# Kernel optimization log

Hardware: AMD Instinct MI355X
Metric: run time of the kernel (lower is better)

## Reference

```python
import jax, jax.numpy as jnp
import numpy as np

D_MODEL = 1024
NUM_HEADS = 16
B, S = 2, 2048


def setup_inputs() -> dict:
    key = jax.random.key(0)
    ks = jax.random.split(key, 11)
    scale = 1.0 / np.sqrt(D_MODEL)
    inp = {
        'q': jax.random.normal(ks[0], (B, S, D_MODEL), jnp.float32),
        'k': jax.random.normal(ks[1], (B, S, D_MODEL), jnp.float32),
        'v': jax.random.normal(ks[2], (B, S, D_MODEL), jnp.float32),
        'w_q': jax.random.normal(ks[3], (D_MODEL, D_MODEL), jnp.float32) * scale,
        'b_q': jax.random.normal(ks[4], (D_MODEL,), jnp.float32) * 0.01,
        'w_k': jax.random.normal(ks[5], (D_MODEL, D_MODEL), jnp.float32) * scale,
        'b_k': jax.random.normal(ks[6], (D_MODEL,), jnp.float32) * 0.01,
        'w_v': jax.random.normal(ks[7], (D_MODEL, D_MODEL), jnp.float32) * scale,
        'b_v': jax.random.normal(ks[8], (D_MODEL,), jnp.float32) * 0.01,
        'w_o': jax.random.normal(ks[9], (D_MODEL, D_MODEL), jnp.float32) * scale,
        'b_o': jax.random.normal(ks[10], (D_MODEL,), jnp.float32) * 0.01,
    }
    return inp


def reference(q, k, v, w_q, b_q, w_k, b_k, w_v, b_v, w_o, b_o):
    Bq, Sq, D = q.shape
    H = NUM_HEADS
    dh = D // H
    # projections (weights stored as [in, out])
    query = q @ w_q + b_q
    key = k @ w_k + b_k
    value = v @ w_v + b_v
    # [B, S, D] -> [B, H, S, dh]
    query = query.reshape(Bq, Sq, H, dh).transpose(0, 2, 1, 3)
    key = key.reshape(Bq, -1, H, dh).transpose(0, 2, 1, 3)
    value = value.reshape(Bq, -1, H, dh).transpose(0, 2, 1, 3)
    # NOTE: original module does NOT scale by 1/sqrt(dh)
    scores = jnp.einsum('bhqd,bhkd->bhqk', query, key)  # [B,H,S,S]
    causal_mask = jnp.triu(jnp.ones((Sq, Sq), dtype=bool), k=1)  # True above diag
    scores = jnp.where(causal_mask[None, None], -jnp.inf, scores)
    attn = jax.nn.softmax(scores, axis=-1)
    data = jnp.einsum('bhqk,bhkd->bhqd', attn, value)  # [B,H,S,dh]
    # FAITHFUL to original bug: transpose(0,1) then view(B, S, -1)
    data = data.transpose(1, 0, 2, 3).reshape(Bq, Sq, -1)  # [H,B,S,dh] -> [B,S,D]
    return data @ w_o + b_o
```

## Files before the change

kernel.cpp:

```cpp
#include <hip/hip_runtime.h>

typedef __fp16 f16;
typedef __fp16 f16x8 __attribute__((ext_vector_type(8)));
typedef __fp16 f16x4 __attribute__((ext_vector_type(4)));
typedef __fp16 f16x2 __attribute__((ext_vector_type(2)));
typedef float f32x4 __attribute__((ext_vector_type(4)));
typedef float f32x16 __attribute__((ext_vector_type(16)));

#define D_MODEL 1024
#define SEQ 2048
#define NH 16
#define MTOT 4096

typedef const __attribute__((address_space(1))) unsigned int* gp1_t;
typedef __attribute__((address_space(3))) unsigned int* lp3_t;

__device__ __forceinline__ void gload_lds16(const void* g, void* l) {
  __builtin_amdgcn_global_load_lds((gp1_t)g, (lp3_t)l, 16, 0, 0);
}

__device__ __forceinline__ int permrow(int r) {
  int bp = r >> 11, u = (r >> 7) & 15, t = r & 127;
  int g16 = (bp << 4) | u;
  return ((((g16 & 1) << 4) | (g16 >> 1)) << 7) + t;
}

__device__ __forceinline__ unsigned int pkrtz(float a, float b) {
  union { f16x2 h; unsigned int u; } z;
  z.h = __builtin_amdgcn_cvt_pkrtz(a, b);
  return z.u;
}

__global__ __launch_bounds__(256) void cvt_all(const float* __restrict__ q,
                                               const float* __restrict__ k,
                                               const float* __restrict__ v,
                                               const float* __restrict__ wq,
                                               const float* __restrict__ wk,
                                               const float* __restrict__ wv,
                                               const float* __restrict__ wo,
                                               f16* __restrict__ qkv16,
                                               f16* __restrict__ wT) {
  __shared__ float tl[64][65];
  int bid = blockIdx.x, tid = threadIdx.x;
  if (bid < 6144) {
    int i = bid * 256 + tid;
    const int NT = (MTOT * D_MODEL) / 8;
    const float* src;
    int t;
    if (i < NT) { src = q; t = i; }
    else if (i < 2 * NT) { src = k; t = i - NT; }
    else { src = v; t = i - 2 * NT; }
    const float4* s4 = (const float4*)src;
    float4 a = s4[2 * t], b = s4[2 * t + 1];
    f16x8 h;
    h[0] = (f16)a.x; h[1] = (f16)a.y; h[2] = (f16)a.z; h[3] = (f16)a.w;
    h[4] = (f16)b.x; h[5] = (f16)b.y; h[6] = (f16)b.z; h[7] = (f16)b.w;
    *(f16x8*)(qkv16 + (size_t)i * 8) = h;
  } else {
    int bb = bid - 6144;
    int mat = bb >> 8, tile = bb & 255;
    int tk = (tile >> 4) << 6, tn = (tile & 15) << 6;
    const float* W = mat == 0 ? wq : mat == 1 ? wk : mat == 2 ? wv : wo;
    int rr = tid >> 4, c4 = (tid & 15) << 2;
#pragma unroll
    for (int it = 0; it < 4; ++it) {
      const float* p = W + (size_t)(tk + it * 16 + rr) * D_MODEL + tn + c4;
      float4 val = *(const float4*)p;
      tl[it * 16 + rr][c4 + 0] = val.x;
      tl[it * 16 + rr][c4 + 1] = val.y;
      tl[it * 16 + rr][c4 + 2] = val.z;
      tl[it * 16 + rr][c4 + 3] = val.w;
    }
    __syncthreads();
    int n = tid & 63, kseg = (tid >> 6) << 4;
    f16x8 lo, hi;
#pragma unroll
    for (int j = 0; j < 8; ++j) lo[j] = (f16)tl[kseg + j][n];
#pragma unroll
    for (int j = 0; j < 8; ++j) hi[j] = (f16)tl[kseg + 8 + j][n];
    f16* d = wT + (size_t)mat * (D_MODEL * D_MODEL) + (size_t)(tn + n) * D_MODEL + tk + kseg;
    *(f16x8*)d = lo;
    *(f16x8*)(d + 8) = hi;
  }
}

#define SLOT_Q 8192
__global__ __launch_bounds__(256, 2) void gemm_qkv(const f16* __restrict__ q16,
                                                   const f16* __restrict__ k16,
                                                   const f16* __restrict__ v16,
                                                   const f16* __restrict__ wT,
                                                   const float* __restrict__ bq,
                                                   const float* __restrict__ bk,
                                                   const float* __restrict__ bv,
                                                   f16* __restrict__ Q16,
                                                   f16* __restrict__ K16,
                                                   f16* __restrict__ VT16) {
  extern __shared__ __attribute__((aligned(16))) f16 sm[];
  const int K = D_MODEL, N = D_MODEL;
  const size_t WEL = (size_t)D_MODEL * D_MODEL;
  int z = blockIdx.z;
  const f16* A = z == 0 ? q16 : z == 1 ? k16 : v16;
  const f16* BT = wT + (size_t)z * WEL;
  const float* bias = z == 0 ? bq : z == 1 ? bk : bv;

  int tid = threadIdx.x;
  int w = tid >> 6, lane = tid & 63;
  int g = lane >> 4, c = lane & 15;
  int wr = w >> 1, wc = w & 1;
  int m0 = blockIdx.x * 128, n0 = blockIdx.y * 128;
  f32x4 acc[4][4] = {};

  int sl0 = lane >> 3, s = lane & 7;
  int u = s ^ sl0;
  int rlow = u >> 2, gsl = u & 3;
  const f16* Agp = A + (size_t)(m0 + w * 32 + 2 * sl0 + rlow) * K + gsl * 8;
  const f16* Bgp = BT + (size_t)(n0 + w * 32 + 2 * sl0 + rlow) * K + gsl * 8;

#define STAGE_Q(tt, bi)                                                      \
  {                                                                          \
    f16* dA = sm + (bi)*SLOT_Q + w * 1024;                                   \
    f16* dB = sm + (bi)*SLOT_Q + 4096 + w * 1024;                            \
    const f16* sa = Agp + (size_t)(tt)*32;                                   \
    const f16* sb = Bgp + (size_t)(tt)*32;                                   \
    gload_lds16(sa, dA);                                                     \
    gload_lds16(sa + (size_t)16 * K, dA + 512);                              \
    gload_lds16(sb, dB);                                                     \
    gload_lds16(sb + (size_t)16 * K, dB + 512);                              \
  }

  STAGE_Q(0, 0)
  STAGE_Q(1, 1)
  STAGE_Q(2, 2)

  const int NKT = K / 32;
  for (int t = 0; t < NKT; ++t) {
    if (t < NKT - 2) asm volatile("s_waitcnt vmcnt(8)" ::: "memory");
    else if (t == NKT - 2) asm volatile("s_waitcnt vmcnt(4)" ::: "memory");
    else asm volatile("s_waitcnt vmcnt(0)" ::: "memory");
    __builtin_amdgcn_sched_barrier(0);
    __builtin_amdgcn_s_barrier();
    __builtin_amdgcn_sched_barrier(0);
    if (t + 3 < NKT) STAGE_Q(t + 3, (t + 3) & 3)

    const char* Ac = (const char*)(sm + (t & 3) * SLOT_Q);
    const char* Bc = Ac + 8192;
    f16x8 af[4], bf[4];
#pragma unroll
    for (int mi = 0; mi < 4; ++mi) {
      int row = wr * 64 + mi * 16 + c;
      int tb = (row >> 1) * 128 + (((((row & 1) << 2) | g) ^ ((row >> 1) & 7)) << 4);
      af[mi] = *(const f16x8*)(Ac + tb);
    }
#pragma unroll
    for (int ni = 0; ni < 4; ++ni) {
      int row = wc * 64 + ni * 16 + c;
      int tb = (row >> 1) * 128 + (((((row & 1) << 2) | g) ^ ((row >> 1) & 7)) << 4);
      bf[ni] = *(const f16x8*)(Bc + tb);
    }
    asm volatile("s_waitcnt lgkmcnt(0)" ::: "memory");
    __builtin_amdgcn_sched_barrier(0);
    __builtin_amdgcn_s_setprio(1);
#pragma unroll
    for (int mi = 0; mi < 4; ++mi)
#pragma unroll
      for (int ni = 0; ni < 4; ++ni)
        acc[mi][ni] = __builtin_amdgcn_mfma_f32_16x16x32_f16(af[mi], bf[ni], acc[mi][ni], 0, 0, 0);
    __builtin_amdgcn_s_setprio(0);
  }

  int rb = m0 + wr * 64;
  int cb = n0 + wc * 64;
  if (z < 2) {
    f16* O = z == 0 ? Q16 : K16;
#pragma unroll
    for (int m = 0; m < 4; ++m) {
      int row0 = rb + m * 16 + 4 * g;
#pragma unroll
      for (int n = 0; n < 4; ++n) {
        int col = cb + n * 16 + c;
        float bv2 = bias[col];
#pragma unroll
        for (int r = 0; r < 4; ++r) O[(size_t)(row0 + r) * N + col] = (f16)(acc[m][n][r] + bv2);
      }
    }
  } else {
    f16* O = VT16;
#pragma unroll
    for (int m = 0; m < 4; ++m) {
      int s0f = rb + m * 16 + 4 * g;
      int bb = s0f >> 11, ss = s0f & (SEQ - 1);
#pragma unroll
      for (int n = 0; n < 4; ++n) {
        int col = cb + n * 16 + c;
        float bv2 = bias[col];
        f16x4 hv;
#pragma unroll
        for (int r = 0; r < 4; ++r) hv[r] = (f16)(acc[m][n][r] + bv2);
        *(f16x4*)(O + ((size_t)(bb * NH + (col >> 6)) * 64 + (col & 63)) * SEQ + ss) = hv;
      }
    }
  }
}

__global__ __launch_bounds__(256, 2) void gemm_out(const f16* __restrict__ A,
                                                   const f16* __restrict__ BT,
                                                   const float* __restrict__ bias,
                                                   float* __restrict__ O) {
  const int K = D_MODEL, N = D_MODEL;
  __shared__ f16 As[64 * 64];
  __shared__ f16 Bs[128 * 64];
  int tid = threadIdx.x;
  int w = tid >> 6, lane = tid & 63;
  int g = lane >> 4, c = lane & 15;
  int wr = w >> 1, wc = w & 1;
  int m0 = blockIdx.x * 64, n0 = blockIdx.y * 128;
  f32x4 acc[2][4] = {};

  for (int kt = 0; kt < K; kt += 64) {
#pragma unroll
    for (int i = 0; i < 2; ++i) {
      int seg = w * 2 + i;
      int p = seg * 1024 + lane * 16;
      int row = p >> 7;
      int colb = (p & 127) ^ ((row & 7) << 4);
      int ae = kt + (colb >> 1);
      gload_lds16(A + (size_t)permrow(m0 + row) * K + ae, &As[seg * 512]);
    }
#pragma unroll
    for (int i = 0; i < 4; ++i) {
      int seg = w * 4 + i;
      int p = seg * 1024 + lane * 16;
      int row = p >> 7;
      int colb = (p & 127) ^ ((row & 7) << 4);
      int ae = kt + (colb >> 1);
      gload_lds16(BT + (size_t)(n0 + row) * K + ae, &Bs[seg * 512]);
    }
    __syncthreads();
    f16x8 af[2][2], bf[4][2];
#pragma unroll
    for (int m = 0; m < 2; ++m) {
#pragma unroll
      for (int kk = 0; kk < 2; ++kk) {
        int row = wr * 32 + m * 16 + c;
        int tb = (row * 128 + kk * 64 + g * 16) ^ ((row & 7) << 4);
        af[m][kk] = *(const f16x8*)((const char*)As + tb);
      }
    }
#pragma unroll
    for (int n = 0; n < 4; ++n) {
#pragma unroll
      for (int kk = 0; kk < 2; ++kk) {
        int row = wc * 64 + n * 16 + c;
        int tb = (row * 128 + kk * 64 + g * 16) ^ ((row & 7) << 4);
        bf[n][kk] = *(const f16x8*)((const char*)Bs + tb);
      }
    }
    __builtin_amdgcn_s_setprio(1);
#pragma unroll
    for (int m = 0; m < 2; ++m)
#pragma unroll
      for (int n = 0; n < 4; ++n)
#pragma unroll
        for (int kk = 0; kk < 2; ++kk)
          acc[m][n] = __builtin_amdgcn_mfma_f32_16x16x32_f16(af[m][kk], bf[n][kk], acc[m][n], 0, 0, 0);
    __builtin_amdgcn_s_setprio(0);
    __syncthreads();
  }

  int rb = m0 + wr * 32;
  int cb = n0 + wc * 64;
#pragma unroll
  for (int m = 0; m < 2; ++m) {
    int row0 = rb + m * 16 + 4 * g;
#pragma unroll
    for (int n = 0; n < 4; ++n) {
      int col = cb + n * 16 + c;
      float bv = bias[col];
#pragma unroll
      for (int r = 0; r < 4; ++r) O[(size_t)(row0 + r) * N + col] = acc[m][n][r] + bv;
    }
  }
}

#define THR2 11.5f
__global__ __launch_bounds__(256, 2) void attn_kernel(const f16* __restrict__ Q,
                                                      const f16* __restrict__ K,
                                                      const f16* __restrict__ VT,
                                                      f16* __restrict__ AO) {
  __shared__ __attribute__((aligned(16))) f16 Ksh[2][2][64 * 64];
  __shared__ __attribute__((aligned(16))) f16 Vsh[2][2][64 * 64];
  const int BUFO = 2 * 64 * 64;
  int tid = threadIdx.x;
  int w = tid >> 6, lane = tid & 63;
  int c = lane & 31, hi = lane >> 5;
  int qh = w & 1, par = w >> 1;
  int blk = blockIdx.x;
  int bh = blk & 31;
  int uu = blk >> 5;
  int cb = 31 - uu;
  int b = bh >> 4, h = bh & 15;
  int q0 = cb * 64 + qh * 32;
  const int NT = cb + 1;
  const size_t brow = (size_t)b * SEQ;
  const int hcol = h * 64;

  int sr = lane >> 3;
  int seo = ((lane & 7) ^ sr) << 3;
  const f16* Kgb = K + (size_t)(brow + qh * 32 + sr) * D_MODEL + hcol + seo;
  const f16* Vgb = VT + ((size_t)bh * 64 + qh * 32 + sr) * SEQ + seo;
  f16* Kshf = &Ksh[0][0][0];
  f16* Vshf = &Vsh[0][0][0];
  f16* KshW = Kshf + par * 4096 + qh * 32 * 64;
  f16* VshW = Vshf + par * 4096 + qh * 32 * 64;

  const f16 LOG2E = (f16)1.44269504f;
  f16x8 qf[4];
  const f16* Qp = Q + (size_t)(brow + q0 + c) * D_MODEL + hcol + 8 * hi;
#pragma unroll
  for (int kk = 0; kk < 4; ++kk) {
    qf[kk] = *(const f16x8*)(Qp + 16 * kk);
#pragma unroll
    for (int j = 0; j < 8; ++j) qf[kk][j] = (f16)(qf[kk][j] * LOG2E);
  }

  float m_st = -1e30f, l_st = 0.f;
  f32x16 o0 = {}, o1 = {};

  if (par < NT) {
    int kv = par * 64;
#pragma unroll
    for (int j = 0; j < 4; ++j) {
      gload_lds16(Kgb + (size_t)(kv + j * 8) * D_MODEL, KshW + (j * 8) * 64);
      gload_lds16(Vgb + (size_t)(j * 8) * SEQ + kv, VshW + (j * 8) * 64);
    }
  }
  __syncthreads();

  int rsw = (c & 7) << 4;
  int cur = 0;
  const int U = (NT + 1) >> 1;
  for (int u = 0; u < U; ++u) {
    int tpre = 2 * u + 2 + par;
    if (tpre < NT) {
      int kv = tpre * 64;
      f16* kd = KshW + (cur ^ 1) * BUFO;
      f16* vd = VshW + (cur ^ 1) * BUFO;
#pragma unroll
      for (int j = 0; j < 4; ++j) {
        gload_lds16(Kgb + (size_t)(kv + j * 8) * D_MODEL, kd + (j * 8) * 64);
        gload_lds16(Vgb + (size_t)(j * 8) * SEQ + kv, vd + (j * 8) * 64);
      }
    }
    int t = 2 * u + par;
    if (t < NT) {
      const char* Kb = (const char*)(Kshf + cur * BUFO + par * 4096);
      const char* Vb = (const char*)(Vshf + cur * BUFO + par * 4096);
      f16x8 kf[2][4];
#pragma unroll
      for (int ks = 0; ks < 2; ++ks)
#pragma unroll
        for (int kk = 0; kk < 4; ++kk)
          kf[ks][kk] = *(const f16x8*)(Kb + (((ks * 32 + c) * 128 + 32 * kk + 16 * hi) ^ rsw));
      f32x16 s0 = {}, s1 = {};
      __builtin_amdgcn_s_setprio(1);
#pragma unroll
      for (int kk = 0; kk < 4; ++kk) {
        s0 = __builtin_amdgcn_mfma_f32_32x32x16_f16(kf[0][kk], qf[kk], s0, 0, 0, 0);
        s1 = __builtin_amdgcn_mfma_f32_32x32x16_f16(kf[1][kk], qf[kk], s1, 0, 0, 0);
      }
      __builtin_amdgcn_s_setprio(0);
      f16x8 vf[2][4];
#pragma unroll
      for (int dt = 0; dt < 2; ++dt)
#pragma unroll
        for (int kk = 0; kk < 4; ++kk)
          vf[dt][kk] = *(const f16x8*)(Vb + (((dt * 32 + c) * 128 + 32 * kk + 16 * hi) ^ rsw));
      if (t == NT - 1) {
        int q = q0 + c;
        int kvb = t * 64 + 4 * hi;
#pragma unroll
        for (int r = 0; r < 16; ++r) {
          int kv = kvb + (r & 3) + 8 * (r >> 2);
          if (kv > q) s0[r] = -1e30f;
          if (kv + 32 > q) s1[r] = -1e30f;
        }
      }
      float t8[8];
#pragma unroll
      for (int r = 0; r < 8; ++r)
        t8[r] = fmaxf(fmaxf(s0[r], s0[r + 8]), fmaxf(s1[r], s1[r + 8]));
      float pm = fmaxf(fmaxf(fmaxf(t8[0], t8[1]), fmaxf(t8[2], t8[3])),
                       fmaxf(fmaxf(t8[4], t8[5]), fmaxf(t8[6], t8[7])));
      float mx = fmaxf(pm, __shfl_xor(pm, 32));
      if (__any(mx > m_st + THR2)) {
        float mnew = fmaxf(m_st, mx);
        float corr = __builtin_amdgcn_exp2f(m_st - mnew);
        l_st *= corr;
#pragma unroll
        for (int r = 0; r < 16; ++r) { o0[r] *= corr; o1[r] *= corr; }
        m_st = mnew;
      }
      float ts[16];
#pragma unroll
      for (int r = 0; r < 16; ++r) {
        float p0 = __builtin_amdgcn_exp2f(s0[r] - m_st);
        float p1 = __builtin_amdgcn_exp2f(s1[r] - m_st);
        s0[r] = p0; s1[r] = p1;
        ts[r] = p0 + p1;
      }
#pragma unroll
      for (int st = 8; st > 0; st >>= 1)
#pragma unroll
        for (int r = 0; r < st; ++r) ts[r] += ts[r + st];
      l_st += ts[0];
      union PU { unsigned int u[4]; f16x8 v; };
      PU pu[4];
#pragma unroll
      for (int kk = 0; kk < 4; ++kk) {
        int rb = 8 * (kk & 1);
        unsigned int la0, la1, lb0, lb1;
        if (kk < 2) {
          la0 = pkrtz(s0[rb + 0], s0[rb + 1]);
          la1 = pkrtz(s0[rb + 2], s0[rb + 3]);
          lb0 = pkrtz(s0[rb + 4], s0[rb + 5]);
          lb1 = pkrtz(s0[rb + 6], s0[rb + 7]);
        } else {
          la0 = pkrtz(s1[rb + 0], s1[rb + 1]);
          la1 = pkrtz(s1[rb + 2], s1[rb + 3]);
          lb0 = pkrtz(s1[rb + 4], s1[rb + 5]);
          lb1 = pkrtz(s1[rb + 6], s1[rb + 7]);
        }
        asm("v_permlane32_swap_b32 %0, %1" : "+v"(la0), "+v"(lb0));
        asm("v_permlane32_swap_b32 %0, %1" : "+v"(la1), "+v"(lb1));
        pu[kk].u[0] = la0; pu[kk].u[1] = la1; pu[kk].u[2] = lb0; pu[kk].u[3] = lb1;
      }
      __builtin_amdgcn_s_setprio(1);
#pragma unroll
      for (int kk = 0; kk < 4; ++kk) {
        o0 = __builtin_amdgcn_mfma_f32_32x32x16_f16(vf[0][kk], pu[kk].v, o0, 0, 0, 0);
        o1 = __builtin_amdgcn_mfma_f32_32x32x16_f16(vf[1][kk], pu[kk].v, o1, 0, 0, 0);
      }
      __builtin_amdgcn_s_setprio(0);
    }
    __syncthreads();
    cur ^= 1;
  }

  float* sc = (float*)Kshf;
  int mb = (qh * 64 + lane) * 34;
  if (par == 1) {
    sc[mb] = m_st;
    sc[mb + 1] = l_st;
#pragma unroll
    for (int r = 0; r < 16; ++r) { sc[mb + 2 + r] = o0[r]; sc[mb + 18 + r] = o1[r]; }
  }
  __syncthreads();
  if (par == 0) {
    float m1 = sc[mb], l1 = sc[mb + 1];
    float mm = fmaxf(m_st, m1);
    float c0 = __builtin_amdgcn_exp2f(m_st - mm);
    float c1 = __builtin_amdgcn_exp2f(m1 - mm);
    float l = l_st * c0 + l1 * c1;
#pragma unroll
    for (int r = 0; r < 16; ++r) {
      o0[r] = o0[r] * c0 + sc[mb + 2 + r] * c1;
      o1[r] = o1[r] * c0 + sc[mb + 18 + r] * c1;
    }
    float lt = l + __shfl_xor(l, 32);
    float linv = 1.0f / lt;
    f16* aoq = AO + ((size_t)bh * SEQ + q0 + c) * 64 + 4 * hi;
#pragma unroll
    for (int rq = 0; rq < 4; ++rq) {
      f16x4 h0, h1;
#pragma unroll
      for (int r = 0; r < 4; ++r) {
        h0[r] = (f16)(o0[4 * rq + r] * linv);
        h1[r] = (f16)(o1[4 * rq + r] * linv);
      }
      *(f16x4*)(aoq + 8 * rq) = h0;
      *(f16x4*)(aoq + 32 + 8 * rq) = h1;
    }
  }
}

extern "C" void kernel_launch(void* const* d_in, const int* in_sizes, int n_in,
                              void* d_out, int out_size, void* d_ws, size_t ws_size,
                              hipStream_t stream) {
  const float* q  = (const float*)d_in[0];
  const float* k  = (const float*)d_in[1];
  const float* v  = (const float*)d_in[2];
  const float* wq = (const float*)d_in[3];
  const float* bq = (const float*)d_in[4];
  const float* wk = (const float*)d_in[5];
  const float* bk = (const float*)d_in[6];
  const float* wv = (const float*)d_in[7];
  const float* bv = (const float*)d_in[8];
  const float* wo = (const float*)d_in[9];
  const float* bo = (const float*)d_in[10];

  const size_t TEN = (size_t)MTOT * D_MODEL;
  const size_t WEL = (size_t)D_MODEL * D_MODEL;
  f16* ws  = (f16*)d_ws;
  f16* q16 = ws;
  f16* k16 = q16 + TEN;
  f16* v16 = k16 + TEN;
  f16* wT  = v16 + TEN;
  f16* Q16 = wT + 4 * WEL;
  f16* K16 = Q16 + TEN;
  f16* VT16 = K16 + TEN;
  f16* AO  = q16;

  static bool attr_set = false;
  if (!attr_set) {
    hipFuncSetAttribute(reinterpret_cast<const void*>(&gemm_qkv),
                        hipFuncAttributeMaxDynamicSharedMemorySize, 65536);
    attr_set = true;
  }

  cvt_all<<<7168, 256, 0, stream>>>(q, k, v, wq, wk, wv, wo, q16, wT);
  gemm_qkv<<<dim3(32, 8, 3), 256, 65536, stream>>>(q16, k16, v16, wT, bq, bk, bv, Q16, K16, VT16);
  attn_kernel<<<1024, 256, 0, stream>>>(Q16, K16, VT16, AO);
  gemm_out<<<dim3(64, 8), 256, 0, stream>>>(AO, wT + 3 * WEL, bo, (float*)d_out);
}
```

Measured before the change: 108.4 us.

## Load K/V fragments directly from global memory, dropping LDS double buffering

The attention kernel no longer stages K and V tiles through double-buffered shared memory with async global-to-LDS loads and per-iteration barriers. Each wave now reads its K and V MFMA fragments straight from global memory (relying on L2/L1 for reuse across the two q-half waves), and only a small float scratch array remains for the final merge. Launch bounds are raised to allow three blocks per CU. In exchange, K/V reuse across waves becomes redundant global traffic and load latency is no longer hidden by explicit prefetching.

```diff
diff --git a/kernel.cpp b/kernel.cpp
--- a/kernel.cpp
+++ b/kernel.cpp
@@ -283,13 +283,11 @@
 }
 
 #define THR2 11.5f
-__global__ __launch_bounds__(256, 2) void attn_kernel(const f16* __restrict__ Q,
+__global__ __launch_bounds__(256, 3) void attn_kernel(const f16* __restrict__ Q,
                                                       const f16* __restrict__ K,
                                                       const f16* __restrict__ VT,
                                                       f16* __restrict__ AO) {
-  __shared__ __attribute__((aligned(16))) f16 Ksh[2][2][64 * 64];
-  __shared__ __attribute__((aligned(16))) f16 Vsh[2][2][64 * 64];
-  const int BUFO = 2 * 64 * 64;
+  __shared__ float sc[128 * 34];
   int tid = threadIdx.x;
   int w = tid >> 6, lane = tid & 63;
   int c = lane & 31, hi = lane >> 5;
@@ -304,14 +302,8 @@
   const size_t brow = (size_t)b * SEQ;
   const int hcol = h * 64;
 
-  int sr = lane >> 3;
-  int seo = ((lane & 7) ^ sr) << 3;
-  const f16* Kgb = K + (size_t)(brow + qh * 32 + sr) * D_MODEL + hcol + seo;
-  const f16* Vgb = VT + ((size_t)bh * 64 + qh * 32 + sr) * SEQ + seo;
-  f16* Kshf = &Ksh[0][0][0];
-  f16* Vshf = &Vsh[0][0][0];
-  f16* KshW = Kshf + par * 4096 + qh * 32 * 64;
-  f16* VshW = Vshf + par * 4096 + qh * 32 * 64;
+  const f16* Kl = K + (size_t)(brow + c) * D_MODEL + hcol + 8 * hi;
+  const f16* Vl = VT + ((size_t)bh * 64 + c) * SEQ + 8 * hi;
 
   const f16 LOG2E = (f16)1.44269504f;
   f16x8 qf[4];
@@ -326,127 +318,99 @@
   float m_st = -1e30f, l_st = 0.f;
   f32x16 o0 = {}, o1 = {};
 
-  if (par < NT) {
-    int kv = par * 64;
-#pragma unroll
-    for (int j = 0; j < 4; ++j) {
-      gload_lds16(Kgb + (size_t)(kv + j * 8) * D_MODEL, KshW + (j * 8) * 64);
-      gload_lds16(Vgb + (size_t)(j * 8) * SEQ + kv, VshW + (j * 8) * 64);
-    }
-  }
-  __syncthreads();
-
-  int rsw = (c & 7) << 4;
-  int cur = 0;
-  const int U = (NT + 1) >> 1;
-  for (int u = 0; u < U; ++u) {
-    int tpre = 2 * u + 2 + par;
-    if (tpre < NT) {
-      int kv = tpre * 64;
-      f16* kd = KshW + (cur ^ 1) * BUFO;
-      f16* vd = VshW + (cur ^ 1) * BUFO;
-#pragma unroll
-      for (int j = 0; j < 4; ++j) {
-        gload_lds16(Kgb + (size_t)(kv + j * 8) * D_MODEL, kd + (j * 8) * 64);
-        gload_lds16(Vgb + (size_t)(j * 8) * SEQ + kv, vd + (j * 8) * 64);
-      }
-    }
-    int t = 2 * u + par;
-    if (t < NT) {
-      const char* Kb = (const char*)(Kshf + cur * BUFO + par * 4096);
-      const char* Vb = (const char*)(Vshf + cur * BUFO + par * 4096);
-      f16x8 kf[2][4];
-#pragma unroll
-      for (int ks = 0; ks < 2; ++ks)
-#pragma unroll
-        for (int kk = 0; kk < 4; ++kk)
-          kf[ks][kk] = *(const f16x8*)(Kb + (((ks * 32 + c) * 128 + 32 * kk + 16 * hi) ^ rsw));
-      f32x16 s0 = {}, s1 = {};
-      __builtin_amdgcn_s_setprio(1);
-#pragma unroll
-      for (int kk = 0; kk < 4; ++kk) {
-        s0 = __builtin_amdgcn_mfma_f32_32x32x16_f16(kf[0][kk], qf[kk], s0, 0, 0, 0);
-        s1 = __builtin_amdgcn_mfma_f32_32x32x16_f16(kf[1][kk], qf[kk], s1, 0, 0, 0);
-      }
-      __builtin_amdgcn_s_setprio(0);
-      f16x8 vf[2][4];
-#pragma unroll
-      for (int dt = 0; dt < 2; ++dt)
-#pragma unroll
-        for (int kk = 0; kk < 4; ++kk)
-          vf[dt][kk] = *(const f16x8*)(Vb + (((dt * 32 + c) * 128 + 32 * kk + 16 * hi) ^ rsw));
-      if (t == NT - 1) {
-        int q = q0 + c;
-        int kvb = t * 64 + 4 * hi;
-#pragma unroll
-        for (int r = 0; r < 16; ++r) {
-          int kv = kvb + (r & 3) + 8 * (r >> 2);
-          if (kv > q) s0[r] = -1e30f;
-          if (kv + 32 > q) s1[r] = -1e30f;
-        }
-      }
-      float t8[8];
-#pragma unroll
-      for (int r = 0; r < 8; ++r)
-        t8[r] = fmaxf(fmaxf(s0[r], s0[r + 8]), fmaxf(s1[r], s1[r + 8]));
-      float pm = fmaxf(fmaxf(fmaxf(t8[0], t8[1]), fmaxf(t8[2], t8[3])),
-                       fmaxf(fmaxf(t8[4], t8[5]), fmaxf(t8[6], t8[7])));
-      float mx = fmaxf(pm, __shfl_xor(pm, 32));
-      if (__any(mx > m_st + THR2)) {
-        float mnew = fmaxf(m_st, mx);
-        float corr = __builtin_amdgcn_exp2f(m_st - mnew);
-        l_st *= corr;
-#pragma unroll
-        for (int r = 0; r < 16; ++r) { o0[r] *= corr; o1[r] *= corr; }
-        m_st = mnew;
-      }
-      float ts[16];
+  for (int t = par; t < NT; t += 2) {
+    int kv0 = t * 64;
+    const f16* K0 = Kl + (size_t)kv0 * D_MODEL;
+    const f16* K1 = K0 + (size_t)32 * D_MODEL;
+    const f16* V0 = Vl + kv0;
+    const f16* V1 = V0 + (size_t)32 * SEQ;
+    f16x8 kf[2][4], vf[2][4];
+#pragma unroll
+    for (int kk = 0; kk < 4; ++kk) {
+      kf[0][kk] = *(const f16x8*)(K0 + 16 * kk);
+      kf[1][kk] = *(const f16x8*)(K1 + 16 * kk);
+    }
+#pragma unroll
+    for (int kk = 0; kk < 4; ++kk) {
+      vf[0][kk] = *(const f16x8*)(V0 + 16 * kk);
+      vf[1][kk] = *(const f16x8*)(V1 + 16 * kk);
+    }
+    f32x16 s0 = {}, s1 = {};
+    __builtin_amdgcn_s_setprio(1);
+#pragma unroll
+    for (int kk = 0; kk < 4; ++kk) {
+      s0 = __builtin_amdgcn_mfma_f32_32x32x16_f16(kf[0][kk], qf[kk], s0, 0, 0, 0);
+      s1 = __builtin_amdgcn_mfma_f32_32x32x16_f16(kf[1][kk], qf[kk], s1, 0, 0, 0);
+    }
+    __builtin_amdgcn_s_setprio(0);
+    if (t == NT - 1) {
+      int q = q0 + c;
+      int kvb = t * 64 + 4 * hi;
 #pragma unroll
       for (int r = 0; r < 16; ++r) {
-        float p0 = __builtin_amdgcn_exp2f(s0[r] - m_st);
-        float p1 = __builtin_amdgcn_exp2f(s1[r] - m_st);
-        s0[r] = p0; s1[r] = p1;
-        ts[r] = p0 + p1;
-      }
-#pragma unroll
-      for (int st = 8; st > 0; st >>= 1)
-#pragma unroll
-        for (int r = 0; r < st; ++r) ts[r] += ts[r + st];
-      l_st += ts[0];
-      union PU { unsigned int u[4]; f16x8 v; };
-      PU pu[4];
-#pragma unroll
-      for (int kk = 0; kk < 4; ++kk) {
-        int rb = 8 * (kk & 1);
-        unsigned int la0, la1, lb0, lb1;
-        if (kk < 2) {
-          la0 = pkrtz(s0[rb + 0], s0[rb + 1]);
-          la1 = pkrtz(s0[rb + 2], s0[rb + 3]);
-          lb0 = pkrtz(s0[rb + 4], s0[rb + 5]);
-          lb1 = pkrtz(s0[rb + 6], s0[rb + 7]);
-        } else {
-          la0 = pkrtz(s1[rb + 0], s1[rb + 1]);
-          la1 = pkrtz(s1[rb + 2], s1[rb + 3]);
-          lb0 = pkrtz(s1[rb + 4], s1[rb + 5]);
-          lb1 = pkrtz(s1[rb + 6], s1[rb + 7]);
-        }
-        asm("v_permlane32_swap_b32 %0, %1" : "+v"(la0), "+v"(lb0));
-        asm("v_permlane32_swap_b32 %0, %1" : "+v"(la1), "+v"(lb1));
-        pu[kk].u[0] = la0; pu[kk].u[1] = la1; pu[kk].u[2] = lb0; pu[kk].u[3] = lb1;
-      }
-      __builtin_amdgcn_s_setprio(1);
-#pragma unroll
-      for (int kk = 0; kk < 4; ++kk) {
-        o0 = __builtin_amdgcn_mfma_f32_32x32x16_f16(vf[0][kk], pu[kk].v, o0, 0, 0, 0);
-        o1 = __builtin_amdgcn_mfma_f32_32x32x16_f16(vf[1][kk], pu[kk].v, o1, 0, 0, 0);
-      }
-      __builtin_amdgcn_s_setprio(0);
-    }
-    __syncthreads();
-    cur ^= 1;
-  }
-
-  float* sc = (float*)Kshf;
+        int kv = kvb + (r & 3) + 8 * (r >> 2);
+        if (kv > q) s0[r] = -1e30f;
+        if (kv + 32 > q) s1[r] = -1e30f;
+      }
+    }
+    float t8[8];
+#pragma unroll
+    for (int r = 0; r < 8; ++r)
+      t8[r] = fmaxf(fmaxf(s0[r], s0[r + 8]), fmaxf(s1[r], s1[r + 8]));
+    float pm = fmaxf(fmaxf(fmaxf(t8[0], t8[1]), fmaxf(t8[2], t8[3])),
+                     fmaxf(fmaxf(t8[4], t8[5]), fmaxf(t8[6], t8[7])));
+    float mx = fmaxf(pm, __shfl_xor(pm, 32));
+    if (__any(mx > m_st + THR2)) {
+      float mnew = fmaxf(m_st, mx);
+      float corr = __builtin_amdgcn_exp2f(m_st - mnew);
+      l_st *= corr;
+#pragma unroll
+      for (int r = 0; r < 16; ++r) { o0[r] *= corr; o1[r] *= corr; }
+      m_st = mnew;
+    }
+    float ts[16];
+#pragma unroll
+    for (int r = 0; r < 16; ++r) {
+      float p0 = __builtin_amdgcn_exp2f(s0[r] - m_st);
+      float p1 = __builtin_amdgcn_exp2f(s1[r] - m_st);
+      s0[r] = p0; s1[r] = p1;
+      ts[r] = p0 + p1;
+    }
+#pragma unroll
+    for (int st = 8; st > 0; st >>= 1)
+#pragma unroll
+      for (int r = 0; r < st; ++r) ts[r] += ts[r + st];
+    l_st += ts[0];
+    union PU { unsigned int u[4]; f16x8 v; };
+    PU pu[4];
+#pragma unroll
+    for (int kk = 0; kk < 4; ++kk) {
+      int rb = 8 * (kk & 1);
+      unsigned int la0, la1, lb0, lb1;
+      if (kk < 2) {
+        la0 = pkrtz(s0[rb + 0], s0[rb + 1]);
+        la1 = pkrtz(s0[rb + 2], s0[rb + 3]);
+        lb0 = pkrtz(s0[rb + 4], s0[rb + 5]);
+        lb1 = pkrtz(s0[rb + 6], s0[rb + 7]);
+      } else {
+        la0 = pkrtz(s1[rb + 0], s1[rb + 1]);
+        la1 = pkrtz(s1[rb + 2], s1[rb + 3]);
+        lb0 = pkrtz(s1[rb + 4], s1[rb + 5]);
+        lb1 = pkrtz(s1[rb + 6], s1[rb + 7]);
+      }
+      asm("v_permlane32_swap_b32 %0, %1" : "+v"(la0), "+v"(lb0));
+      asm("v_permlane32_swap_b32 %0, %1" : "+v"(la1), "+v"(lb1));
+      pu[kk].u[0] = la0; pu[kk].u[1] = la1; pu[kk].u[2] = lb0; pu[kk].u[3] = lb1;
+    }
+    __builtin_amdgcn_s_setprio(1);
+#pragma unroll
+    for (int kk = 0; kk < 4; ++kk) {
+      o0 = __builtin_amdgcn_mfma_f32_32x32x16_f16(vf[0][kk], pu[kk].v, o0, 0, 0, 0);
+      o1 = __builtin_amdgcn_mfma_f32_32x32x16_f16(vf[1][kk], pu[kk].v, o1, 0, 0, 0);
+    }
+    __builtin_amdgcn_s_setprio(0);
+  }
+
   int mb = (qh * 64 + lane) * 34;
   if (par == 1) {
     sc[mb] = m_st;
```

Measured after the change: 144.0 us. 1.33x slower.

## Enlarge attention blocks to 128 query rows with 8 waves sharing K/V tiles

Applied to the files above, without the earlier changes.

The attention kernel now processes 128 query rows per block with 512 threads (four query sub-tiles by two KV parities) instead of 64 rows with 256 threads. Each K/V tile staged in LDS is shared by more waves, and the grid drops to 512 blocks. Blocks are ordered so long and short causal blocks are paired for load balance. Waves whose diagonal tile is earlier skip compute, which leaves some idle time inside the larger blocks and puts more pressure on LDS and registers per CU.

```diff
diff --git a/kernel.cpp b/kernel.cpp
--- a/kernel.cpp
+++ b/kernel.cpp
@@ -283,35 +283,36 @@
 }
 
 #define THR2 11.5f
-__global__ __launch_bounds__(256, 2) void attn_kernel(const f16* __restrict__ Q,
+__global__ __launch_bounds__(512, 4) void attn_kernel(const f16* __restrict__ Q,
                                                       const f16* __restrict__ K,
                                                       const f16* __restrict__ VT,
                                                       f16* __restrict__ AO) {
-  __shared__ __attribute__((aligned(16))) f16 Ksh[2][2][64 * 64];
-  __shared__ __attribute__((aligned(16))) f16 Vsh[2][2][64 * 64];
-  const int BUFO = 2 * 64 * 64;
+  __shared__ __attribute__((aligned(16))) f16 SM[32768];
+  const int BUFO = 2 * 4096;
   int tid = threadIdx.x;
   int w = tid >> 6, lane = tid & 63;
   int c = lane & 31, hi = lane >> 5;
-  int qh = w & 1, par = w >> 1;
+  int qh = w & 3, par = w >> 2;
   int blk = blockIdx.x;
   int bh = blk & 31;
   int uu = blk >> 5;
-  int cb = 31 - uu;
+  int cb = (blk < 256) ? (15 - uu) : (uu - 8);
   int b = bh >> 4, h = bh & 15;
-  int q0 = cb * 64 + qh * 32;
-  const int NT = cb + 1;
+  int q0 = cb * 128 + qh * 32;
+  const int NT = 2 * cb + 2;
+  const int U = cb + 1;
+  const int dg = 2 * cb + (qh >> 1);
   const size_t brow = (size_t)b * SEQ;
   const int hcol = h * 64;
 
   int sr = lane >> 3;
   int seo = ((lane & 7) ^ sr) << 3;
-  const f16* Kgb = K + (size_t)(brow + qh * 32 + sr) * D_MODEL + hcol + seo;
-  const f16* Vgb = VT + ((size_t)bh * 64 + qh * 32 + sr) * SEQ + seo;
-  f16* Kshf = &Ksh[0][0][0];
-  f16* Vshf = &Vsh[0][0][0];
-  f16* KshW = Kshf + par * 4096 + qh * 32 * 64;
-  f16* VshW = Vshf + par * 4096 + qh * 32 * 64;
+  const f16* Kgb = K + (size_t)(brow + qh * 16 + sr) * D_MODEL + hcol + seo;
+  const f16* Vgb = VT + ((size_t)bh * 64 + qh * 16 + sr) * SEQ + seo;
+  f16* Kshf = SM;
+  f16* Vshf = SM + 16384;
+  f16* KshW = Kshf + par * 4096 + qh * 16 * 64;
+  f16* VshW = Vshf + par * 4096 + qh * 16 * 64;
 
   const f16 LOG2E = (f16)1.44269504f;
   f16x8 qf[4];
@@ -326,10 +327,10 @@
   float m_st = -1e30f, l_st = 0.f;
   f32x16 o0 = {}, o1 = {};
 
-  if (par < NT) {
+  {
     int kv = par * 64;
 #pragma unroll
-    for (int j = 0; j < 4; ++j) {
+    for (int j = 0; j < 2; ++j) {
       gload_lds16(Kgb + (size_t)(kv + j * 8) * D_MODEL, KshW + (j * 8) * 64);
       gload_lds16(Vgb + (size_t)(j * 8) * SEQ + kv, VshW + (j * 8) * 64);
     }
@@ -338,21 +339,20 @@
 
   int rsw = (c & 7) << 4;
   int cur = 0;
-  const int U = (NT + 1) >> 1;
-  for (int u = 0; u < U; ++u) {
-    int tpre = 2 * u + 2 + par;
+  for (int idx = 0; idx < U; ++idx) {
+    int t = 2 * idx + par;
+    int tpre = t + 2;
     if (tpre < NT) {
       int kv = tpre * 64;
       f16* kd = KshW + (cur ^ 1) * BUFO;
       f16* vd = VshW + (cur ^ 1) * BUFO;
 #pragma unroll
-      for (int j = 0; j < 4; ++j) {
+      for (int j = 0; j < 2; ++j) {
         gload_lds16(Kgb + (size_t)(kv + j * 8) * D_MODEL, kd + (j * 8) * 64);
         gload_lds16(Vgb + (size_t)(j * 8) * SEQ + kv, vd + (j * 8) * 64);
       }
     }
-    int t = 2 * u + par;
-    if (t < NT) {
+    if (t <= dg) {
       const char* Kb = (const char*)(Kshf + cur * BUFO + par * 4096);
       const char* Vb = (const char*)(Vshf + cur * BUFO + par * 4096);
       f16x8 kf[2][4];
@@ -375,7 +375,7 @@
 #pragma unroll
         for (int kk = 0; kk < 4; ++kk)
           vf[dt][kk] = *(const f16x8*)(Vb + (((dt * 32 + c) * 128 + 32 * kk + 16 * hi) ^ rsw));
-      if (t == NT - 1) {
+      if (t == dg) {
         int q = q0 + c;
         int kvb = t * 64 + 4 * hi;
 #pragma unroll
@@ -446,7 +446,7 @@
     cur ^= 1;
   }
 
-  float* sc = (float*)Kshf;
+  float* sc = (float*)SM;
   int mb = (qh * 64 + lane) * 34;
   if (par == 1) {
     sc[mb] = m_st;
@@ -519,6 +519,6 @@
 
   cvt_all<<<7168, 256, 0, stream>>>(q, k, v, wq, wk, wv, wo, q16, wT);
   gemm_qkv<<<dim3(32, 8, 3), 256, 65536, stream>>>(q16, k16, v16, wT, bq, bk, bv, Q16, K16, VT16);
-  attn_kernel<<<1024, 256, 0, stream>>>(Q16, K16, VT16, AO);
+  attn_kernel<<<512, 512, 0, stream>>>(Q16, K16, VT16, AO);
   gemm_out<<<dim3(64, 8), 256, 0, stream>>>(AO, wT + 3 * WEL, bo, (float*)d_out);
 }
```

Result: slower. 124.6 us (+14.9%).
